# Performance work log

Measured on AMD Instinct MI355X. Metric: run time of the kernel, lower is better.

The kernel has to match this reference:

```python
import jax, jax.numpy as jnp
import numpy as np

LEAK = 0.2
TEMP = 0.1          # CausalMask temperature
SPARSITY_W = 0.1
MI_W = 0.01
DAG_W = 1.0

def _leaky(x):
    return jax.nn.leaky_relu(x, LEAK)

def setup_inputs() -> dict:
    key = jax.random.key(0)
    B, F, S, H = 4096, 512, 32, 512
    H2, CH = H // 2, 64
    P = S * (S - 1) // 2  # 496 MI estimators
    ks = jax.random.split(key, 32)
    def w(k, shape, fan_in):
        return jax.random.normal(k, shape, jnp.float32) / np.sqrt(fan_in)
    return {
        'features': jax.random.normal(ks[0], (B, F), jnp.float32),
        'eps':      jax.random.normal(ks[1], (B, S), jnp.float32),
        'enc_w1': w(ks[2], (F, H), F),   'enc_b1': w(ks[3], (H,), H),
        'enc_w2': w(ks[4], (H, 2 * S), H), 'enc_b2': w(ks[5], (2 * S,), H) * 0.1,
        'log_weight': jax.random.normal(ks[6], (S, S), jnp.float32) * 0.5,
        'mech_w1': w(ks[7], (S, S, H2), S), 'mech_b1': w(ks[8], (S, H2), H2),
        'mech_w2': w(ks[9], (S, H2), H2),   'mech_b2': w(ks[10], (S,), H2),
        'dec_w1': w(ks[11], (S, H), S),  'dec_b1': w(ks[12], (H,), H),
        'dec_w2': w(ks[13], (H, F), H),  'dec_b2': w(ks[14], (F,), H),
        'mi_w1': w(ks[15], (P, 2, CH), 2),  'mi_b1': w(ks[16], (P, CH), CH),
        'mi_w2': w(ks[17], (P, CH, CH), CH), 'mi_b2': w(ks[18], (P, CH), CH),
        'mi_w3': w(ks[19], (P, CH), CH),     'mi_b3': w(ks[20], (P,), CH),
    }

def _forward(features, eps, enc_w1, enc_b1, enc_w2, enc_b2, log_weight,
             mech_w1, mech_b1, mech_w2, mech_b2, dec_w1, dec_b1, dec_w2, dec_b2,
             mi_w1, mi_b1, mi_w2, mi_b2, mi_w3, mi_b3):
    S = log_weight.shape[0]
    # ---- encode ----
    h = _leaky(features @ enc_w1 + enc_b1)
    params = h @ enc_w2 + enc_b2
    mean, log_std = jnp.split(params, 2, axis=-1)
    std = jnp.exp(log_std)
    z = mean + std * eps                                   # [B,S]
    # ---- soft causal adjacency (training mode) ----
    eye = jnp.eye(S, dtype=features.dtype)
    upper = jnp.triu(jnp.ones((S, S), features.dtype), k=1)
    lw = log_weight * upper - 10.0 * eye
    A = jax.nn.sigmoid(lw / TEMP)                          # [S,S]
    # ---- apply_causal_structure: stoch_dim tiny MLPs, vectorized ----
    # z_parents[b,i,s] = z[b,s] * A[s,i]
    zp = z[:, None, :] * A.T[None, :, :]                   # [B,S,S]
    h1 = _leaky(jnp.einsum('bis,ish->bih', zp, mech_w1) + mech_b1)  # [B,S,H2]
    z_causal = jnp.einsum('bih,ih->bi', h1, mech_w2) + mech_b2      # [B,S]
    # ---- decode ----
    recon = _leaky(z_causal @ dec_w1 + dec_b1) @ dec_w2 + dec_b2    # [B,F]
    # ---- losses ----
    recon_loss = jnp.mean((recon - features) ** 2)
    kl_loss = 0.5 * jnp.sum(mean ** 2 + std ** 2 - 2.0 * log_std - 1.0, axis=-1).mean()
    Asig = jax.nn.sigmoid(log_weight)
    sparsity_loss = jnp.sum(jnp.abs(Asig))
    # MI: one tiny MLP per (i<j) pair, row-major order == torch loop order
    iu, ju = jnp.triu_indices(S, k=1)
    pair = jnp.stack([z[:, iu], z[:, ju]], axis=-1)        # [B,P,2]
    m1 = _leaky(jnp.einsum('bpi,pih->bph', pair, mi_w1) + mi_b1)
    m2 = _leaky(jnp.einsum('bph,phk->bpk', m1, mi_w2) + mi_b2)
    mi_est = (jnp.einsum('bph,ph->bp', m2, mi_w3) + mi_b3).mean(0)  # [P]
    mi_loss = jnp.sum(jax.nn.sigmoid(log_weight[iu, ju]) * mi_est)
    # DAG: truncated matrix-exponential trace penalty
    A2 = Asig * Asig
    expm = eye
    mp = eye
    fact = 1.0
    for i in range(1, 10):
        fact *= i
        mp = mp @ A2
        expm = expm + mp / fact
    dag_loss = (jnp.trace(expm) - S) ** 2
    total_loss = recon_loss + kl_loss + SPARSITY_W * sparsity_loss + MI_W * mi_loss + DAG_W * dag_loss
    return z_causal, mean, std, recon, total_loss, recon_loss, kl_loss, sparsity_loss, mi_loss, dag_loss

def reference(features, eps, enc_w1, enc_b1, enc_w2, enc_b2, log_weight,
              mech_w1, mech_b1, mech_w2, mech_b2, dec_w1, dec_b1, dec_w2, dec_b2,
              mi_w1, mi_b1, mi_w2, mi_b2, mi_w3, mi_b3):
    return _forward(features, eps, enc_w1, enc_b1, enc_w2, enc_b2, log_weight,
                    mech_w1, mech_b1, mech_w2, mech_b2, dec_w1, dec_b1, dec_w2, dec_b2,
                    mi_w1, mi_b1, mi_w2, mi_b2, mi_w3, mi_b3)
```

## Files before the change

kernel.cpp:

```cpp
#include <hip/hip_runtime.h>
#include <hip/hip_bf16.h>

typedef float f32x4 __attribute__((ext_vector_type(4)));
typedef short s16x8 __attribute__((ext_vector_type(8)));

__device__ __forceinline__ float leaky2(float x){ return fmaf(0.4f, fabsf(x), 0.6f * x); }

__device__ __forceinline__ short f2bf(float f){
    return __builtin_bit_cast(short, __float2bfloat16(f));
}

__global__ __launch_bounds__(256) void k_cvt(
    const float* __restrict__ feat, const float* __restrict__ ew1,
    const float* __restrict__ ew2, const float* __restrict__ dw2,
    const float* __restrict__ mw1, const float* __restrict__ mw2,
    short* __restrict__ featbf, short* __restrict__ w1p,
    short* __restrict__ ew2p, short* __restrict__ dw2p,
    short* __restrict__ mw1p, short* __restrict__ mw2p,
    const float* __restrict__ lw, float* __restrict__ A,
    float* __restrict__ acc)
{
    if (blockIdx.x >= 2048){
        __shared__ float A2s[1024], mp[1024], red[256];
        const int t = threadIdx.x;
        float part = 0.f;
        #pragma unroll
        for (int q = 0; q < 4; ++q){
            int e = t * 4 + q;
            int r = e >> 5, c = e & 31;
            float v = lw[e];
            float sig = 1.f / (1.f + expf(-v));
            float l2 = (r < c) ? v * 10.f : ((r == c) ? -100.f : 0.f);
            A[e] = 1.f / (1.f + expf(-l2));
            part += sig;
            float a2 = sig * sig;
            A2s[e] = a2; mp[e] = a2;
        }
        red[t] = part; __syncthreads();
        for (int s = 128; s > 0; s >>= 1){ if (t < s) red[t] += red[t + s]; __syncthreads(); }
        if (t == 0) acc[2] = red[0];

        const float invf[10] = {0.f, 1.f, 0.5f, 1.6666667e-1f, 4.1666667e-2f,
                                8.3333333e-3f, 1.3888889e-3f, 1.9841270e-4f,
                                2.4801587e-5f, 2.7557319e-6f};
        float tr = 0.f;
        const int r = t >> 3, c0 = (t & 7) * 4;
        for (int n = 1; n <= 9; ++n){
            __syncthreads();
            if (t == 0){
                float s = 0.f;
                for (int k2 = 0; k2 < 32; ++k2) s += mp[k2 * 33];
                tr += s * invf[n];
            }
            if (n == 9) break;
            float av[4] = {0.f, 0.f, 0.f, 0.f};
            for (int k2 = 0; k2 < 32; ++k2){
                float m = mp[r * 32 + k2];
                #pragma unroll
                for (int q = 0; q < 4; ++q) av[q] = fmaf(m, A2s[k2 * 32 + c0 + q], av[q]);
            }
            __syncthreads();
            #pragma unroll
            for (int q = 0; q < 4; ++q) mp[r * 32 + c0 + q] = av[q];
        }
        if (t == 0) acc[3] = tr * tr;
        return;
    }
    for (int idx = blockIdx.x * 256 + threadIdx.x; idx < 4947968; idx += 2048 * 256){
        if (idx < 2097152){ featbf[idx] = f2bf(feat[idx]); continue; }
        int s = idx - 2097152;
        if (s < 262144){
            int k = s >> 9, n = s & 511;
            int lane = (((k >> 3) & 3) << 4) | (n & 15);
            w1p[((n >> 4) * 16 + (k >> 5)) * 512 + lane * 8 + (k & 7)] = f2bf(ew1[s]);
            continue;
        }
        s -= 262144;
        if (s < 32768){
            int k = s >> 6, n = s & 63;
            int lane = (((k >> 3) & 3) << 4) | (n & 15);
            ew2p[((n >> 4) * 16 + (k >> 5)) * 512 + lane * 8 + (k & 7)] = f2bf(ew2[s]);
            continue;
        }
        s -= 32768;
        if (s < 262144){
            int k = s >> 9, n = s & 511;
            int lane = (((k >> 3) & 3) << 4) | (n & 15);
            dw2p[((n >> 4) * 16 + (k >> 5)) * 512 + lane * 8 + (k & 7)] = f2bf(dw2[s]);
            continue;
        }
        s -= 262144;
        if (s < 262144){
            int i = s >> 13, r2 = s & 8191;
            int k = r2 >> 8, n = r2 & 255;
            int lane = (((k >> 3) & 3) << 4) | (n & 15);
            mw1p[i * 8192 + (n >> 4) * 512 + lane * 8 + (k & 7)] = f2bf(mw1[s]);
            continue;
        }
        s -= 262144;
        int p = s >> 12, r2 = s & 4095;
        int k = r2 >> 6, n = r2 & 63;
        int lane = (((k >> 3) & 3) << 4) | (n & 15);
        mw2p[p * 4096 + ((n >> 4) * 2 + (k >> 5)) * 512 + lane * 8 + (k & 7)] = f2bf(mw2[s]);
    }
}

__global__ __launch_bounds__(256) void k_genc(const short* __restrict__ Abf,
                                              const short* __restrict__ Bp,
                                              const float* __restrict__ bias,
                                              short* __restrict__ Hbf)
{
    const int lane = threadIdx.x & 63, wv = threadIdx.x >> 6;
    const int ml = lane & 15, kg = lane >> 4;
    const int b0 = blockIdx.x * 32 + (wv >> 1) * 16;
    const int c0 = blockIdx.y * 128 + (wv & 1) * 64;
    const int nt0 = c0 >> 4;
    f32x4 acc[4] = {};
    for (int kt = 0; kt < 16; ++kt){
        s16x8 a = *(const s16x8*)&Abf[(size_t)(b0 + ml) * 512 + kt * 32 + kg * 8];
        #pragma unroll
        for (int ni = 0; ni < 4; ++ni){
            s16x8 b = *(const s16x8*)&Bp[((nt0 + ni) * 16 + kt) * 512 + lane * 8];
            acc[ni] = __builtin_amdgcn_mfma_f32_16x16x32_bf16(a, b, acc[ni], 0, 0, 0);
        }
    }
    #pragma unroll
    for (int ni = 0; ni < 4; ++ni){
        int col = c0 + ni * 16 + ml;
        float bv = bias[col];
        #pragma unroll
        for (int r = 0; r < 4; ++r){
            int row = b0 + kg * 4 + r;
            Hbf[(size_t)row * 512 + col] = f2bf(leaky2(acc[ni][r] + bv));
        }
    }
}

__global__ __launch_bounds__(256) void k_grec(const short* __restrict__ Abf,
                                              const short* __restrict__ Bp,
                                              const float* __restrict__ bias,
                                              const float* __restrict__ feat,
                                              float* __restrict__ recon,
                                              float* __restrict__ accg)
{
    __shared__ float red[256];
    const int t = threadIdx.x;
    const int lane = t & 63, wv = t >> 6;
    const int ml = lane & 15, kg = lane >> 4;
    const int b0 = blockIdx.x * 32 + (wv >> 1) * 16;
    const int c0 = blockIdx.y * 128 + (wv & 1) * 64;
    const int nt0 = c0 >> 4;
    f32x4 acc[4] = {};
    for (int kt = 0; kt < 16; ++kt){
        s16x8 a = *(const s16x8*)&Abf[(size_t)(b0 + ml) * 512 + kt * 32 + kg * 8];
        #pragma unroll
        for (int ni = 0; ni < 4; ++ni){
            s16x8 b = *(const s16x8*)&Bp[((nt0 + ni) * 16 + kt) * 512 + lane * 8];
            acc[ni] = __builtin_amdgcn_mfma_f32_16x16x32_bf16(a, b, acc[ni], 0, 0, 0);
        }
    }
    float lsum = 0.f;
    #pragma unroll
    for (int ni = 0; ni < 4; ++ni){
        int col = c0 + ni * 16 + ml;
        float bv = bias[col];
        #pragma unroll
        for (int r = 0; r < 4; ++r){
            int row = b0 + kg * 4 + r;
            float v = acc[ni][r] + bv;
            float d = v - feat[(size_t)row * 512 + col];
            lsum = fmaf(d, d, lsum);
            recon[(size_t)row * 512 + col] = v;
        }
    }
    red[t] = lsum; __syncthreads();
    for (int s = 128; s > 0; s >>= 1){ if (t < s) red[t] += red[t + s]; __syncthreads(); }
    if (t == 0) atomicAdd(accg + 1, red[0]);
}

__global__ __launch_bounds__(256) void k_pmfma(const short* __restrict__ Hbf,
                                               const short* __restrict__ Bp,
                                               const float* __restrict__ b2,
                                               const float* __restrict__ eps,
                                               float* __restrict__ omean,
                                               float* __restrict__ ostd,
                                               float* __restrict__ zt,
                                               float* __restrict__ accg)
{
    __shared__ float P[16][65];
    __shared__ float zs[16][33];
    __shared__ float red[256];
    const int t = threadIdx.x, lane = t & 63, wv = t >> 6;
    const int ml = lane & 15, kg = lane >> 4;
    const int b0 = blockIdx.x * 16;
    f32x4 acc = {};
    for (int kt = 0; kt < 16; ++kt){
        s16x8 b = *(const s16x8*)&Bp[(wv * 16 + kt) * 512 + lane * 8];
        s16x8 a = *(const s16x8*)&Hbf[(size_t)(b0 + ml) * 512 + kt * 32 + kg * 8];
        acc = __builtin_amdgcn_mfma_f32_16x16x32_bf16(a, b, acc, 0, 0, 0);
    }
    {
        int col = wv * 16 + ml;
        float bv = b2[col];
        #pragma unroll
        for (int r = 0; r < 4; ++r)
            P[kg * 4 + r][col] = acc[r] + bv;
    }
    __syncthreads();
    float klp = 0.f;
    #pragma unroll
    for (int q = 0; q < 2; ++q){
        int e = q * 256 + t;
        int row = e >> 5, n = e & 31;
        float mean = P[row][n], ls = P[row][n + 32];
        float sd = expf(ls);
        size_t o = (size_t)(b0 + row) * 32 + n;
        float z = fmaf(sd, eps[o], mean);
        omean[o] = mean; ostd[o] = sd;
        zs[row][n] = z;
        klp += mean * mean + sd * sd - 2.f * ls - 1.f;
    }
    __syncthreads();
    #pragma unroll
    for (int q = 0; q < 2; ++q){
        int e = q * 256 + t;
        int n = e >> 4, row = e & 15;
        zt[(size_t)n * 4096 + b0 + row] = zs[row][n];
    }
    red[t] = klp; __syncthreads();
    for (int s = 128; s > 0; s >>= 1){ if (t < s) red[t] += red[t + s]; __syncthreads(); }
    if (t == 0) atomicAdd(accg + 0, red[0]);
}

__global__ __launch_bounds__(256) void k_mi(
    const float* __restrict__ zt,
    const float* __restrict__ w1g, const float* __restrict__ b1g,
    const short* __restrict__ w2p, const float* __restrict__ b2g,
    const float* __restrict__ w3g, float* __restrict__ macc)
{
    const int lane = threadIdx.x & 63, wv = threadIdx.x >> 6;
    const int ml = lane & 15, kg = lane >> 4;
    const int p = blockIdx.x >> 2, bq = blockIdx.x & 3;
    int pi = 0, rem = p;
    while (rem >= 31 - pi){ rem -= 31 - pi; ++pi; }
    const int pj = pi + 1 + rem;

    const int zrow = wv * 16 + ml;
    const float* zi_b = zt + (size_t)pi * 4096 + bq * 1024 + zrow;
    const float* zj_b = zt + (size_t)pj * 4096 + bq * 1024 + zrow;

    float w10s[2][8], w11s[2][8], b1s[2][8];
    #pragma unroll
    for (int ks = 0; ks < 2; ++ks)
        #pragma unroll
        for (int i2 = 0; i2 < 8; ++i2){
            int h = ks * 32 + kg * 8 + i2;
            w10s[ks][i2] = 0.6f * w1g[p * 128 + h];
            w11s[ks][i2] = 0.6f * w1g[p * 128 + 64 + h];
            b1s[ks][i2]  = 0.6f * b1g[p * 64 + h];
        }
    s16x8 bfr[4][2];
    f32x4 b2c[4];
    #pragma unroll
    for (int nb = 0; nb < 4; ++nb){
        float bv = b2g[p * 64 + nb * 16 + ml];
        b2c[nb][0] = bv; b2c[nb][1] = bv; b2c[nb][2] = bv; b2c[nb][3] = bv;
        #pragma unroll
        for (int ks = 0; ks < 2; ++ks)
            bfr[nb][ks] = *(const s16x8*)&w2p[(size_t)p * 4096 + (nb * 2 + ks) * 512 + lane * 8];
    }
    float slin[4] = {0.f, 0.f, 0.f, 0.f}, sabs[4] = {0.f, 0.f, 0.f, 0.f};
    float zi_c = zi_b[0], zj_c = zj_b[0];
    #pragma unroll 1
    for (int tile = 0; tile < 16; ++tile){
        int nx = (tile < 15 ? tile + 1 : 15) * 64;
        float zi_n = zi_b[nx], zj_n = zj_b[nx];
        s16x8 af0, af1;
        #pragma unroll
        for (int i2 = 0; i2 < 8; ++i2){
            float m0 = fmaf(zi_c, w10s[0][i2], fmaf(zj_c, w11s[0][i2], b1s[0][i2]));
            m0 = fmaf(0.66666669f, fabsf(m0), m0);
            af0[i2] = f2bf(m0);
            float m1 = fmaf(zi_c, w10s[1][i2], fmaf(zj_c, w11s[1][i2], b1s[1][i2]));
            m1 = fmaf(0.66666669f, fabsf(m1), m1);
            af1[i2] = f2bf(m1);
        }
        #pragma unroll
        for (int nb = 0; nb < 4; ++nb){
            f32x4 d = __builtin_amdgcn_mfma_f32_16x16x32_bf16(af0, bfr[nb][0], b2c[nb], 0, 0, 0);
            d = __builtin_amdgcn_mfma_f32_16x16x32_bf16(af1, bfr[nb][1], d, 0, 0, 0);
            #pragma unroll
            for (int r2 = 0; r2 < 4; ++r2){
                slin[nb] += d[r2];
                sabs[nb] += fabsf(d[r2]);
            }
        }
        zi_c = zi_n; zj_c = zj_n;
    }
    float s = 0.f;
    #pragma unroll
    for (int nb = 0; nb < 4; ++nb){
        float w3 = w3g[p * 64 + nb * 16 + ml];
        s = fmaf(0.6f * w3, slin[nb], fmaf(0.4f * w3, sabs[nb], s));
    }
    #pragma unroll
    for (int off = 32; off; off >>= 1) s += __shfl_xor(s, off);
    if (lane == 0) atomicAdd(&macc[p], s);
}

__global__ __launch_bounds__(256) void k_mech(
    const float* __restrict__ zt, const float* __restrict__ A,
    const short* __restrict__ W1p, const float* __restrict__ mb1,
    const float* __restrict__ mw2, const float* __restrict__ mb2,
    float* __restrict__ out_zc)
{
    __shared__ float sA[32], sB1[256], sW2[256];
    const int t = threadIdx.x, lane = t & 63, wv = t >> 6;
    const int ml = lane & 15, kg = lane >> 4;
    const int i = blockIdx.y;
    const int b0 = blockIdx.x * 64 + wv * 16;
    if (t < 32) sA[t] = A[t * 32 + i];
    sB1[t] = mb1[i * 256 + t];
    sW2[t] = mw2[i * 256 + t];
    __syncthreads();
    float zv[8];
    #pragma unroll
    for (int q = 0; q < 8; ++q)
        zv[q] = zt[(size_t)(kg * 8 + q) * 4096 + b0 + ml];
    s16x8 af;
    #pragma unroll
    for (int q = 0; q < 8; ++q)
        af[q] = f2bf(zv[q] * sA[kg * 8 + q]);
    float s[4] = {0.f, 0.f, 0.f, 0.f};
    #pragma unroll
    for (int nt = 0; nt < 16; ++nt){
        s16x8 bf = *(const s16x8*)&W1p[i * 8192 + nt * 512 + lane * 8];
        int col = nt * 16 + ml;
        float b1v = sB1[col], w2v = sW2[col];
        f32x4 d;
        d[0] = b1v; d[1] = b1v; d[2] = b1v; d[3] = b1v;
        d = __builtin_amdgcn_mfma_f32_16x16x32_bf16(af, bf, d, 0, 0, 0);
        float w2a = 0.6f * w2v, w2b = 0.4f * w2v;
        #pragma unroll
        for (int r = 0; r < 4; ++r)
            s[r] = fmaf(w2a, d[r], fmaf(w2b, fabsf(d[r]), s[r]));
    }
    #pragma unroll
    for (int off = 1; off < 16; off <<= 1)
        #pragma unroll
        for (int r = 0; r < 4; ++r) s[r] += __shfl_xor(s[r], off);
    if (ml == 0){
        float bb = mb2[i];
        #pragma unroll
        for (int r = 0; r < 4; ++r){
            int b = b0 + kg * 4 + r;
            out_zc[(size_t)b * 32 + i] = s[r] + bb;
        }
    }
}

__global__ __launch_bounds__(256) void k_dec1(
    const float* __restrict__ zc, const float* __restrict__ w1,
    const float* __restrict__ b1, short* __restrict__ d1)
{
    int gid = blockIdx.x * 256 + threadIdx.x;
    int b = gid >> 9, hc = gid & 511;
    const f32x4* z4 = (const f32x4*)(zc + (size_t)b * 32);
    float a = b1[hc];
    #pragma unroll
    for (int q = 0; q < 8; ++q){
        f32x4 v = z4[q];
        a = fmaf(v[0], w1[(q * 4 + 0) * 512 + hc], a);
        a = fmaf(v[1], w1[(q * 4 + 1) * 512 + hc], a);
        a = fmaf(v[2], w1[(q * 4 + 2) * 512 + hc], a);
        a = fmaf(v[3], w1[(q * 4 + 3) * 512 + hc], a);
    }
    d1[(size_t)b * 512 + hc] = f2bf(leaky2(a));
}

__global__ void k_final(const float* __restrict__ acc, const float* __restrict__ lw,
                        const float* __restrict__ b3, float* __restrict__ outs)
{
    __shared__ float red[512];
    int t = threadIdx.x;
    float c = 0.f;
    if (t < 496){
        int pi = 0, rem = t;
        while (rem >= 31 - pi){ rem -= 31 - pi; ++pi; }
        int pj = pi + 1 + rem;
        float est = acc[4 + t] * (1.f / 4096.f) + b3[t];
        float w = 1.f / (1.f + expf(-lw[pi * 32 + pj]));
        c = w * est;
    }
    red[t] = c; __syncthreads();
    for (int s = 256; s > 0; s >>= 1){ if (t < s) red[t] += red[t + s]; __syncthreads(); }
    if (t == 0){
        float mi    = red[0];
        float recon = acc[1] * (1.f / (4096.f * 512.f));
        float kl    = 0.5f * acc[0] * (1.f / 4096.f);
        float sp    = acc[2], dag = acc[3];
        outs[0] = recon + kl + 0.1f * sp + 0.01f * mi + dag;
        outs[1] = recon; outs[2] = kl; outs[3] = sp; outs[4] = mi; outs[5] = dag;
    }
}

extern "C" void kernel_launch(void* const* d_in, const int* in_sizes, int n_in,
                              void* d_out, int out_size, void* d_ws, size_t ws_size,
                              hipStream_t stream)
{
    const float* features = (const float*)d_in[0];
    const float* eps      = (const float*)d_in[1];
    const float* enc_w1   = (const float*)d_in[2];
    const float* enc_b1   = (const float*)d_in[3];
    const float* enc_w2   = (const float*)d_in[4];
    const float* enc_b2   = (const float*)d_in[5];
    const float* log_w    = (const float*)d_in[6];
    const float* mech_w1  = (const float*)d_in[7];
    const float* mech_b1  = (const float*)d_in[8];
    const float* mech_w2  = (const float*)d_in[9];
    const float* mech_b2  = (const float*)d_in[10];
    const float* dec_w1   = (const float*)d_in[11];
    const float* dec_b1   = (const float*)d_in[12];
    const float* dec_w2   = (const float*)d_in[13];
    const float* dec_b2   = (const float*)d_in[14];
    const float* mi_w1    = (const float*)d_in[15];
    const float* mi_b1    = (const float*)d_in[16];
    const float* mi_w2    = (const float*)d_in[17];
    const float* mi_b2    = (const float*)d_in[18];
    const float* mi_w3    = (const float*)d_in[19];
    const float* mi_b3    = (const float*)d_in[20];

    float* W      = (float*)d_ws;
    float* zt     = W;
    float* Abuf   = W + 262144;
    float* accums = W + 263168;
    short* w1p    = (short*)(W + 263680);
    short* ew2p   = (short*)(W + 394752);
    short* dw2p   = (short*)(W + 411136);
    short* mw1p   = (short*)(W + 542208);
    short* d1bf   = (short*)(W + 673280);
    short* mw2p   = d1bf;
    float* out    = (float*)d_out;
    short* featbf = (short*)(out + 393216);
    short* hbf    = (short*)(out + 393216 + 1048576);

    hipMemsetAsync(accums, 0, 512 * sizeof(float), stream);
    k_cvt<<<2049, 256, 0, stream>>>(features, enc_w1, enc_w2, dec_w2, mech_w1, mi_w2,
                                    featbf, w1p, ew2p, dw2p, mw1p, mw2p,
                                    log_w, Abuf, accums);
    k_genc<<<dim3(128, 4), 256, 0, stream>>>(featbf, w1p, enc_b1, hbf);
    k_pmfma<<<256, 256, 0, stream>>>(hbf, ew2p, enc_b2, eps,
                                     out + 131072, out + 262144, zt, accums);
    k_mi<<<1984, 256, 0, stream>>>(zt, mi_w1, mi_b1, mw2p, mi_b2, mi_w3, accums + 4);
    k_mech<<<dim3(64, 32), 256, 0, stream>>>(zt, Abuf, mw1p, mech_b1, mech_w2, mech_b2, out);
    k_dec1<<<8192, 256, 0, stream>>>(out, dec_w1, dec_b1, d1bf);
    k_grec<<<dim3(128, 4), 256, 0, stream>>>(d1bf, dw2p, dec_b2, features,
                                             out + 393216, accums);
    k_final<<<1, 512, 0, stream>>>(accums, log_w, mi_b3, out + 2490368);
}
```

Before: 133.4 us.

## Fuse encoder GEMMs, merge MI and mechanism kernels, fuse decoder into MFMA kernel

Fuses the two encoder GEMMs into one kernel that keeps the hidden activations in swizzled LDS instead of round-tripping them through global memory. The MI estimator and causal-mechanism kernels are merged into one launch using block-index ranges. The decoder's scalar first layer is replaced by an MFMA layer over a prepacked bf16 dec_w1, fused with the second GEMM through LDS. The aim is fewer launches and less intermediate global traffic. In exchange, the fused encoder runs only 256 blocks with 8 accumulators per wave, which lowers parallelism, and the decoder recomputes the hidden layer once per column block (4x redundant).

```diff
diff --git a/kernel.cpp b/kernel.cpp
--- a/kernel.cpp
+++ b/kernel.cpp
@@ -2,6 +2,7 @@
 #include <hip/hip_bf16.h>
 
 typedef float f32x4 __attribute__((ext_vector_type(4)));
+typedef float f32x2 __attribute__((ext_vector_type(2)));
 typedef short s16x8 __attribute__((ext_vector_type(8)));
 
 __device__ __forceinline__ float leaky2(float x){ return fmaf(0.4f, fabsf(x), 0.6f * x); }
@@ -14,9 +15,11 @@
     const float* __restrict__ feat, const float* __restrict__ ew1,
     const float* __restrict__ ew2, const float* __restrict__ dw2,
     const float* __restrict__ mw1, const float* __restrict__ mw2,
+    const float* __restrict__ dw1,
     short* __restrict__ featbf, short* __restrict__ w1p,
     short* __restrict__ ew2p, short* __restrict__ dw2p,
     short* __restrict__ mw1p, short* __restrict__ mw2p,
+    short* __restrict__ dw1p,
     const float* __restrict__ lw, float* __restrict__ A,
     float* __restrict__ acc)
 {
@@ -66,7 +69,7 @@
         if (t == 0) acc[3] = tr * tr;
         return;
     }
-    for (int idx = blockIdx.x * 256 + threadIdx.x; idx < 4947968; idx += 2048 * 256){
+    for (int idx = blockIdx.x * 256 + threadIdx.x; idx < 4964352; idx += 2048 * 256){
         if (idx < 2097152){ featbf[idx] = f2bf(feat[idx]); continue; }
         int s = idx - 2097152;
         if (s < 262144){
@@ -98,113 +101,70 @@
             continue;
         }
         s -= 262144;
-        int p = s >> 12, r2 = s & 4095;
-        int k = r2 >> 6, n = r2 & 63;
+        if (s < 2031616){
+            int p = s >> 12, r2 = s & 4095;
+            int k = r2 >> 6, n = r2 & 63;
+            int lane = (((k >> 3) & 3) << 4) | (n & 15);
+            mw2p[p * 4096 + ((n >> 4) * 2 + (k >> 5)) * 512 + lane * 8 + (k & 7)] = f2bf(mw2[s]);
+            continue;
+        }
+        s -= 2031616;
+        int k = s >> 9, n = s & 511;
         int lane = (((k >> 3) & 3) << 4) | (n & 15);
-        mw2p[p * 4096 + ((n >> 4) * 2 + (k >> 5)) * 512 + lane * 8 + (k & 7)] = f2bf(mw2[s]);
-    }
-}
-
-__global__ __launch_bounds__(256) void k_genc(const short* __restrict__ Abf,
-                                              const short* __restrict__ Bp,
-                                              const float* __restrict__ bias,
-                                              short* __restrict__ Hbf)
-{
-    const int lane = threadIdx.x & 63, wv = threadIdx.x >> 6;
-    const int ml = lane & 15, kg = lane >> 4;
-    const int b0 = blockIdx.x * 32 + (wv >> 1) * 16;
-    const int c0 = blockIdx.y * 128 + (wv & 1) * 64;
-    const int nt0 = c0 >> 4;
-    f32x4 acc[4] = {};
-    for (int kt = 0; kt < 16; ++kt){
-        s16x8 a = *(const s16x8*)&Abf[(size_t)(b0 + ml) * 512 + kt * 32 + kg * 8];
-        #pragma unroll
-        for (int ni = 0; ni < 4; ++ni){
-            s16x8 b = *(const s16x8*)&Bp[((nt0 + ni) * 16 + kt) * 512 + lane * 8];
-            acc[ni] = __builtin_amdgcn_mfma_f32_16x16x32_bf16(a, b, acc[ni], 0, 0, 0);
-        }
-    }
-    #pragma unroll
-    for (int ni = 0; ni < 4; ++ni){
-        int col = c0 + ni * 16 + ml;
-        float bv = bias[col];
-        #pragma unroll
-        for (int r = 0; r < 4; ++r){
-            int row = b0 + kg * 4 + r;
-            Hbf[(size_t)row * 512 + col] = f2bf(leaky2(acc[ni][r] + bv));
-        }
-    }
-}
-
-__global__ __launch_bounds__(256) void k_grec(const short* __restrict__ Abf,
-                                              const short* __restrict__ Bp,
-                                              const float* __restrict__ bias,
-                                              const float* __restrict__ feat,
-                                              float* __restrict__ recon,
-                                              float* __restrict__ accg)
-{
-    __shared__ float red[256];
-    const int t = threadIdx.x;
-    const int lane = t & 63, wv = t >> 6;
-    const int ml = lane & 15, kg = lane >> 4;
-    const int b0 = blockIdx.x * 32 + (wv >> 1) * 16;
-    const int c0 = blockIdx.y * 128 + (wv & 1) * 64;
-    const int nt0 = c0 >> 4;
-    f32x4 acc[4] = {};
-    for (int kt = 0; kt < 16; ++kt){
-        s16x8 a = *(const s16x8*)&Abf[(size_t)(b0 + ml) * 512 + kt * 32 + kg * 8];
-        #pragma unroll
-        for (int ni = 0; ni < 4; ++ni){
-            s16x8 b = *(const s16x8*)&Bp[((nt0 + ni) * 16 + kt) * 512 + lane * 8];
-            acc[ni] = __builtin_amdgcn_mfma_f32_16x16x32_bf16(a, b, acc[ni], 0, 0, 0);
-        }
-    }
-    float lsum = 0.f;
-    #pragma unroll
-    for (int ni = 0; ni < 4; ++ni){
-        int col = c0 + ni * 16 + ml;
-        float bv = bias[col];
-        #pragma unroll
-        for (int r = 0; r < 4; ++r){
-            int row = b0 + kg * 4 + r;
-            float v = acc[ni][r] + bv;
-            float d = v - feat[(size_t)row * 512 + col];
-            lsum = fmaf(d, d, lsum);
-            recon[(size_t)row * 512 + col] = v;
-        }
-    }
-    red[t] = lsum; __syncthreads();
-    for (int s = 128; s > 0; s >>= 1){ if (t < s) red[t] += red[t + s]; __syncthreads(); }
-    if (t == 0) atomicAdd(accg + 1, red[0]);
-}
-
-__global__ __launch_bounds__(256) void k_pmfma(const short* __restrict__ Hbf,
-                                               const short* __restrict__ Bp,
-                                               const float* __restrict__ b2,
-                                               const float* __restrict__ eps,
-                                               float* __restrict__ omean,
-                                               float* __restrict__ ostd,
-                                               float* __restrict__ zt,
-                                               float* __restrict__ accg)
-{
+        dw1p[(n >> 4) * 512 + lane * 8 + (k & 7)] = f2bf(dw1[s]);
+    }
+}
+
+__global__ __launch_bounds__(256) void k_encf(
+    const short* __restrict__ featbf, const short* __restrict__ w1p,
+    const float* __restrict__ eb1, const short* __restrict__ ew2p,
+    const float* __restrict__ eb2, const float* __restrict__ eps,
+    float* __restrict__ omean, float* __restrict__ ostd,
+    float* __restrict__ zt, float* __restrict__ accg)
+{
+    __shared__ short hlds[8192];
     __shared__ float P[16][65];
     __shared__ float zs[16][33];
     __shared__ float red[256];
     const int t = threadIdx.x, lane = t & 63, wv = t >> 6;
     const int ml = lane & 15, kg = lane >> 4;
     const int b0 = blockIdx.x * 16;
-    f32x4 acc = {};
+
+    f32x4 acc1[8] = {};
     for (int kt = 0; kt < 16; ++kt){
-        s16x8 b = *(const s16x8*)&Bp[(wv * 16 + kt) * 512 + lane * 8];
-        s16x8 a = *(const s16x8*)&Hbf[(size_t)(b0 + ml) * 512 + kt * 32 + kg * 8];
-        acc = __builtin_amdgcn_mfma_f32_16x16x32_bf16(a, b, acc, 0, 0, 0);
+        s16x8 a = *(const s16x8*)&featbf[(size_t)(b0 + ml) * 512 + kt * 32 + kg * 8];
+        #pragma unroll
+        for (int nf = 0; nf < 8; ++nf){
+            s16x8 b = *(const s16x8*)&w1p[((wv * 8 + nf) * 16 + kt) * 512 + lane * 8];
+            acc1[nf] = __builtin_amdgcn_mfma_f32_16x16x32_bf16(a, b, acc1[nf], 0, 0, 0);
+        }
+    }
+    #pragma unroll
+    for (int nf = 0; nf < 8; ++nf){
+        int col = wv * 128 + nf * 16 + ml;
+        float bv = eb1[col];
+        #pragma unroll
+        for (int r = 0; r < 4; ++r){
+            int row = kg * 4 + r;
+            int byte = (row * 1024 + col * 2) ^ ((row & 7) << 4);
+            hlds[byte >> 1] = f2bf(leaky2(acc1[nf][r] + bv));
+        }
+    }
+    __syncthreads();
+
+    f32x4 acc2 = {};
+    for (int kt = 0; kt < 16; ++kt){
+        int byte = (ml * 1024 + kt * 64 + kg * 16) ^ ((ml & 7) << 4);
+        s16x8 a = *(const s16x8*)((const char*)hlds + byte);
+        s16x8 b = *(const s16x8*)&ew2p[(wv * 16 + kt) * 512 + lane * 8];
+        acc2 = __builtin_amdgcn_mfma_f32_16x16x32_bf16(a, b, acc2, 0, 0, 0);
     }
     {
         int col = wv * 16 + ml;
-        float bv = b2[col];
+        float bv = eb2[col];
         #pragma unroll
         for (int r = 0; r < 4; ++r)
-            P[kg * 4 + r][col] = acc[r] + bv;
+            P[kg * 4 + r][col] = acc2[r] + bv;
     }
     __syncthreads();
     float klp = 0.f;
@@ -232,150 +192,213 @@
     if (t == 0) atomicAdd(accg + 0, red[0]);
 }
 
-__global__ __launch_bounds__(256) void k_mi(
+__global__ __launch_bounds__(256) void k_mimech(
     const float* __restrict__ zt,
     const float* __restrict__ w1g, const float* __restrict__ b1g,
     const short* __restrict__ w2p, const float* __restrict__ b2g,
-    const float* __restrict__ w3g, float* __restrict__ macc)
-{
-    const int lane = threadIdx.x & 63, wv = threadIdx.x >> 6;
-    const int ml = lane & 15, kg = lane >> 4;
-    const int p = blockIdx.x >> 2, bq = blockIdx.x & 3;
-    int pi = 0, rem = p;
-    while (rem >= 31 - pi){ rem -= 31 - pi; ++pi; }
-    const int pj = pi + 1 + rem;
-
-    const int zrow = wv * 16 + ml;
-    const float* zi_b = zt + (size_t)pi * 4096 + bq * 1024 + zrow;
-    const float* zj_b = zt + (size_t)pj * 4096 + bq * 1024 + zrow;
-
-    float w10s[2][8], w11s[2][8], b1s[2][8];
-    #pragma unroll
-    for (int ks = 0; ks < 2; ++ks)
-        #pragma unroll
-        for (int i2 = 0; i2 < 8; ++i2){
-            int h = ks * 32 + kg * 8 + i2;
-            w10s[ks][i2] = 0.6f * w1g[p * 128 + h];
-            w11s[ks][i2] = 0.6f * w1g[p * 128 + 64 + h];
-            b1s[ks][i2]  = 0.6f * b1g[p * 64 + h];
-        }
-    s16x8 bfr[4][2];
-    f32x4 b2c[4];
-    #pragma unroll
-    for (int nb = 0; nb < 4; ++nb){
-        float bv = b2g[p * 64 + nb * 16 + ml];
-        b2c[nb][0] = bv; b2c[nb][1] = bv; b2c[nb][2] = bv; b2c[nb][3] = bv;
-        #pragma unroll
-        for (int ks = 0; ks < 2; ++ks)
-            bfr[nb][ks] = *(const s16x8*)&w2p[(size_t)p * 4096 + (nb * 2 + ks) * 512 + lane * 8];
-    }
-    float slin[4] = {0.f, 0.f, 0.f, 0.f}, sabs[4] = {0.f, 0.f, 0.f, 0.f};
-    float zi_c = zi_b[0], zj_c = zj_b[0];
-    #pragma unroll 1
-    for (int tile = 0; tile < 16; ++tile){
-        int nx = (tile < 15 ? tile + 1 : 15) * 64;
-        float zi_n = zi_b[nx], zj_n = zj_b[nx];
-        s16x8 af0, af1;
-        #pragma unroll
-        for (int i2 = 0; i2 < 8; ++i2){
-            float m0 = fmaf(zi_c, w10s[0][i2], fmaf(zj_c, w11s[0][i2], b1s[0][i2]));
-            m0 = fmaf(0.66666669f, fabsf(m0), m0);
-            af0[i2] = f2bf(m0);
-            float m1 = fmaf(zi_c, w10s[1][i2], fmaf(zj_c, w11s[1][i2], b1s[1][i2]));
-            m1 = fmaf(0.66666669f, fabsf(m1), m1);
-            af1[i2] = f2bf(m1);
-        }
-        #pragma unroll
-        for (int nb = 0; nb < 4; ++nb){
-            f32x4 d = __builtin_amdgcn_mfma_f32_16x16x32_bf16(af0, bfr[nb][0], b2c[nb], 0, 0, 0);
-            d = __builtin_amdgcn_mfma_f32_16x16x32_bf16(af1, bfr[nb][1], d, 0, 0, 0);
-            #pragma unroll
-            for (int r2 = 0; r2 < 4; ++r2){
-                slin[nb] += d[r2];
-                sabs[nb] += fabsf(d[r2]);
-            }
-        }
-        zi_c = zi_n; zj_c = zj_n;
-    }
-    float s = 0.f;
-    #pragma unroll
-    for (int nb = 0; nb < 4; ++nb){
-        float w3 = w3g[p * 64 + nb * 16 + ml];
-        s = fmaf(0.6f * w3, slin[nb], fmaf(0.4f * w3, sabs[nb], s));
-    }
-    #pragma unroll
-    for (int off = 32; off; off >>= 1) s += __shfl_xor(s, off);
-    if (lane == 0) atomicAdd(&macc[p], s);
-}
-
-__global__ __launch_bounds__(256) void k_mech(
-    const float* __restrict__ zt, const float* __restrict__ A,
-    const short* __restrict__ W1p, const float* __restrict__ mb1,
-    const float* __restrict__ mw2, const float* __restrict__ mb2,
-    float* __restrict__ out_zc)
+    const float* __restrict__ w3g, float* __restrict__ macc,
+    const float* __restrict__ A, const short* __restrict__ W1p,
+    const float* __restrict__ mb1, const float* __restrict__ mw2,
+    const float* __restrict__ mb2, float* __restrict__ out_zc)
 {
     __shared__ float sA[32], sB1[256], sW2[256];
     const int t = threadIdx.x, lane = t & 63, wv = t >> 6;
     const int ml = lane & 15, kg = lane >> 4;
-    const int i = blockIdx.y;
-    const int b0 = blockIdx.x * 64 + wv * 16;
-    if (t < 32) sA[t] = A[t * 32 + i];
-    sB1[t] = mb1[i * 256 + t];
-    sW2[t] = mw2[i * 256 + t];
+    if (blockIdx.x < 1984){
+        const int p = blockIdx.x >> 2, bq = blockIdx.x & 3;
+        int pi = 0, rem = p;
+        while (rem >= 31 - pi){ rem -= 31 - pi; ++pi; }
+        const int pj = pi + 1 + rem;
+
+        const int zrow = wv * 16 + ml;
+        const float* zi_b = zt + (size_t)pi * 4096 + bq * 1024 + zrow;
+        const float* zj_b = zt + (size_t)pj * 4096 + bq * 1024 + zrow;
+
+        f32x2 w10v[2][4], w11v[2][4], b1v[2][4];
+        #pragma unroll
+        for (int ks = 0; ks < 2; ++ks)
+            #pragma unroll
+            for (int q = 0; q < 4; ++q){
+                int h = ks * 32 + kg * 8 + q * 2;
+                w10v[ks][q] = *(const f32x2*)&w1g[p * 128 + h] * 0.6f;
+                w11v[ks][q] = *(const f32x2*)&w1g[p * 128 + 64 + h] * 0.6f;
+                b1v[ks][q]  = *(const f32x2*)&b1g[p * 64 + h] * 0.6f;
+            }
+        s16x8 bfr[4][2];
+        f32x4 b2c[4];
+        #pragma unroll
+        for (int nb = 0; nb < 4; ++nb){
+            float bv = b2g[p * 64 + nb * 16 + ml];
+            b2c[nb][0] = bv; b2c[nb][1] = bv; b2c[nb][2] = bv; b2c[nb][3] = bv;
+            #pragma unroll
+            for (int ks = 0; ks < 2; ++ks)
+                bfr[nb][ks] = *(const s16x8*)&w2p[(size_t)p * 4096 + (nb * 2 + ks) * 512 + lane * 8];
+        }
+        const f32x2 c23 = {0.66666669f, 0.66666669f};
+        float slin[4] = {0.f, 0.f, 0.f, 0.f}, sabs[4] = {0.f, 0.f, 0.f, 0.f};
+        #pragma unroll 1
+        for (int tile = 0; tile < 16; ++tile){
+            float zi_c = zi_b[tile * 64], zj_c = zj_b[tile * 64];
+            f32x2 zi2 = {zi_c, zi_c}, zj2 = {zj_c, zj_c};
+            s16x8 af0, af1;
+            #pragma unroll
+            for (int q = 0; q < 4; ++q){
+                f32x2 m0 = __builtin_elementwise_fma(zi2, w10v[0][q],
+                           __builtin_elementwise_fma(zj2, w11v[0][q], b1v[0][q]));
+                m0 = __builtin_elementwise_fma(c23, __builtin_elementwise_abs(m0), m0);
+                af0[q * 2] = f2bf(m0[0]); af0[q * 2 + 1] = f2bf(m0[1]);
+                f32x2 m1 = __builtin_elementwise_fma(zi2, w10v[1][q],
+                           __builtin_elementwise_fma(zj2, w11v[1][q], b1v[1][q]));
+                m1 = __builtin_elementwise_fma(c23, __builtin_elementwise_abs(m1), m1);
+                af1[q * 2] = f2bf(m1[0]); af1[q * 2 + 1] = f2bf(m1[1]);
+            }
+            #pragma unroll
+            for (int nb = 0; nb < 4; ++nb){
+                f32x4 d = __builtin_amdgcn_mfma_f32_16x16x32_bf16(af0, bfr[nb][0], b2c[nb], 0, 0, 0);
+                d = __builtin_amdgcn_mfma_f32_16x16x32_bf16(af1, bfr[nb][1], d, 0, 0, 0);
+                #pragma unroll
+                for (int r2 = 0; r2 < 4; ++r2){
+                    slin[nb] += d[r2];
+                    sabs[nb] += fabsf(d[r2]);
+                }
+            }
+        }
+        float s = 0.f;
+        #pragma unroll
+        for (int nb = 0; nb < 4; ++nb){
+            float w3 = w3g[p * 64 + nb * 16 + ml];
+            s = fmaf(0.6f * w3, slin[nb], fmaf(0.4f * w3, sabs[nb], s));
+        }
+        #pragma unroll
+        for (int off = 32; off; off >>= 1) s += __shfl_xor(s, off);
+        if (lane == 0) atomicAdd(&macc[p], s);
+    } else {
+        const int bx = blockIdx.x - 1984;
+        const int i = bx & 31;
+        const int b0 = (bx >> 5) * 64 + wv * 16;
+        if (t < 32) sA[t] = A[t * 32 + i];
+        sB1[t] = mb1[i * 256 + t];
+        sW2[t] = mw2[i * 256 + t];
+        __syncthreads();
+        float zv[8];
+        #pragma unroll
+        for (int q = 0; q < 8; ++q)
+            zv[q] = zt[(size_t)(kg * 8 + q) * 4096 + b0 + ml];
+        s16x8 af;
+        #pragma unroll
+        for (int q = 0; q < 8; ++q)
+            af[q] = f2bf(zv[q] * sA[kg * 8 + q]);
+        float s[4] = {0.f, 0.f, 0.f, 0.f};
+        #pragma unroll
+        for (int nt = 0; nt < 16; ++nt){
+            s16x8 bf = *(const s16x8*)&W1p[i * 8192 + nt * 512 + lane * 8];
+            int col = nt * 16 + ml;
+            float b1e = sB1[col], w2v = sW2[col];
+            f32x4 d;
+            d[0] = b1e; d[1] = b1e; d[2] = b1e; d[3] = b1e;
+            d = __builtin_amdgcn_mfma_f32_16x16x32_bf16(af, bf, d, 0, 0, 0);
+            float w2a = 0.6f * w2v, w2b = 0.4f * w2v;
+            #pragma unroll
+            for (int r = 0; r < 4; ++r)
+                s[r] = fmaf(w2a, d[r], fmaf(w2b, fabsf(d[r]), s[r]));
+        }
+        #pragma unroll
+        for (int off = 1; off < 16; off <<= 1)
+            #pragma unroll
+            for (int r = 0; r < 4; ++r) s[r] += __shfl_xor(s[r], off);
+        if (ml == 0){
+            float bb = mb2[i];
+            #pragma unroll
+            for (int r = 0; r < 4; ++r){
+                int b = b0 + kg * 4 + r;
+                out_zc[(size_t)b * 32 + i] = s[r] + bb;
+            }
+        }
+    }
+}
+
+__global__ __launch_bounds__(256) void k_decf(
+    const float* __restrict__ zc, const short* __restrict__ dw1p,
+    const float* __restrict__ db1, const short* __restrict__ dw2p,
+    const float* __restrict__ db2, const float* __restrict__ feat,
+    float* __restrict__ recon, float* __restrict__ accg)
+{
+    __shared__ short dlds[16384];
+    __shared__ float red[256];
+    const int t = threadIdx.x, lane = t & 63, wv = t >> 6;
+    const int ml = lane & 15, kg = lane >> 4;
+    const int b0 = blockIdx.x * 32;
+    const int c0 = blockIdx.y * 128;
+
+    s16x8 af[2];
+    #pragma unroll
+    for (int m = 0; m < 2; ++m){
+        int row = b0 + m * 16 + ml;
+        f32x4 z0 = *(const f32x4*)&zc[(size_t)row * 32 + kg * 8];
+        f32x4 z1 = *(const f32x4*)&zc[(size_t)row * 32 + kg * 8 + 4];
+        #pragma unroll
+        for (int e = 0; e < 4; ++e){
+            af[m][e] = f2bf(z0[e]);
+            af[m][e + 4] = f2bf(z1[e]);
+        }
+    }
+    #pragma unroll
+    for (int nf = 0; nf < 8; ++nf){
+        int nt = wv * 8 + nf;
+        s16x8 bf = *(const s16x8*)&dw1p[nt * 512 + lane * 8];
+        int col = nt * 16 + ml;
+        float b1e = db1[col];
+        f32x4 c; c[0] = b1e; c[1] = b1e; c[2] = b1e; c[3] = b1e;
+        #pragma unroll
+        for (int m = 0; m < 2; ++m){
+            f32x4 d = __builtin_amdgcn_mfma_f32_16x16x32_bf16(af[m], bf, c, 0, 0, 0);
+            #pragma unroll
+            for (int r = 0; r < 4; ++r){
+                int row = m * 16 + kg * 4 + r;
+                int byte = (row * 1024 + col * 2) ^ ((row & 7) << 4);
+                dlds[byte >> 1] = f2bf(leaky2(d[r]));
+            }
+        }
+    }
     __syncthreads();
-    float zv[8];
-    #pragma unroll
-    for (int q = 0; q < 8; ++q)
-        zv[q] = zt[(size_t)(kg * 8 + q) * 4096 + b0 + ml];
-    s16x8 af;
-    #pragma unroll
-    for (int q = 0; q < 8; ++q)
-        af[q] = f2bf(zv[q] * sA[kg * 8 + q]);
-    float s[4] = {0.f, 0.f, 0.f, 0.f};
-    #pragma unroll
-    for (int nt = 0; nt < 16; ++nt){
-        s16x8 bf = *(const s16x8*)&W1p[i * 8192 + nt * 512 + lane * 8];
-        int col = nt * 16 + ml;
-        float b1v = sB1[col], w2v = sW2[col];
-        f32x4 d;
-        d[0] = b1v; d[1] = b1v; d[2] = b1v; d[3] = b1v;
-        d = __builtin_amdgcn_mfma_f32_16x16x32_bf16(af, bf, d, 0, 0, 0);
-        float w2a = 0.6f * w2v, w2b = 0.4f * w2v;
-        #pragma unroll
-        for (int r = 0; r < 4; ++r)
-            s[r] = fmaf(w2a, d[r], fmaf(w2b, fabsf(d[r]), s[r]));
-    }
-    #pragma unroll
-    for (int off = 1; off < 16; off <<= 1)
-        #pragma unroll
-        for (int r = 0; r < 4; ++r) s[r] += __shfl_xor(s[r], off);
-    if (ml == 0){
-        float bb = mb2[i];
-        #pragma unroll
-        for (int r = 0; r < 4; ++r){
-            int b = b0 + kg * 4 + r;
-            out_zc[(size_t)b * 32 + i] = s[r] + bb;
-        }
-    }
-}
-
-__global__ __launch_bounds__(256) void k_dec1(
-    const float* __restrict__ zc, const float* __restrict__ w1,
-    const float* __restrict__ b1, short* __restrict__ d1)
-{
-    int gid = blockIdx.x * 256 + threadIdx.x;
-    int b = gid >> 9, hc = gid & 511;
-    const f32x4* z4 = (const f32x4*)(zc + (size_t)b * 32);
-    float a = b1[hc];
-    #pragma unroll
-    for (int q = 0; q < 8; ++q){
-        f32x4 v = z4[q];
-        a = fmaf(v[0], w1[(q * 4 + 0) * 512 + hc], a);
-        a = fmaf(v[1], w1[(q * 4 + 1) * 512 + hc], a);
-        a = fmaf(v[2], w1[(q * 4 + 2) * 512 + hc], a);
-        a = fmaf(v[3], w1[(q * 4 + 3) * 512 + hc], a);
-    }
-    d1[(size_t)b * 512 + hc] = f2bf(leaky2(a));
+
+    f32x4 acc[2][2] = {};
+    for (int kt = 0; kt < 16; ++kt){
+        s16x8 a[2];
+        #pragma unroll
+        for (int m = 0; m < 2; ++m){
+            int row = m * 16 + ml;
+            int byte = (row * 1024 + kt * 64 + kg * 16) ^ ((row & 7) << 4);
+            a[m] = *(const s16x8*)((const char*)dlds + byte);
+        }
+        #pragma unroll
+        for (int j = 0; j < 2; ++j){
+            int nt = (c0 >> 4) + wv * 2 + j;
+            s16x8 b = *(const s16x8*)&dw2p[(nt * 16 + kt) * 512 + lane * 8];
+            #pragma unroll
+            for (int m = 0; m < 2; ++m)
+                acc[m][j] = __builtin_amdgcn_mfma_f32_16x16x32_bf16(a[m], b, acc[m][j], 0, 0, 0);
+        }
+    }
+    float lsum = 0.f;
+    #pragma unroll
+    for (int j = 0; j < 2; ++j){
+        int col = c0 + (wv * 2 + j) * 16 + ml;
+        float bv = db2[col];
+        #pragma unroll
+        for (int m = 0; m < 2; ++m)
+            #pragma unroll
+            for (int r = 0; r < 4; ++r){
+                int row = b0 + m * 16 + kg * 4 + r;
+                float v = acc[m][j][r] + bv;
+                float d = v - feat[(size_t)row * 512 + col];
+                lsum = fmaf(d, d, lsum);
+                recon[(size_t)row * 512 + col] = v;
+            }
+    }
+    red[t] = lsum; __syncthreads();
+    for (int s = 128; s > 0; s >>= 1){ if (t < s) red[t] += red[t + s]; __syncthreads(); }
+    if (t == 0) atomicAdd(accg + 1, red[0]);
 }
 
 __global__ void k_final(const float* __restrict__ acc, const float* __restrict__ lw,
@@ -438,23 +461,20 @@
     short* ew2p   = (short*)(W + 394752);
     short* dw2p   = (short*)(W + 411136);
     short* mw1p   = (short*)(W + 542208);
-    short* d1bf   = (short*)(W + 673280);
-    short* mw2p   = d1bf;
+    short* mw2p   = (short*)(W + 673280);
+    short* dw1p   = (short*)(W + 1689088);
     float* out    = (float*)d_out;
     short* featbf = (short*)(out + 393216);
-    short* hbf    = (short*)(out + 393216 + 1048576);
 
     hipMemsetAsync(accums, 0, 512 * sizeof(float), stream);
     k_cvt<<<2049, 256, 0, stream>>>(features, enc_w1, enc_w2, dec_w2, mech_w1, mi_w2,
-                                    featbf, w1p, ew2p, dw2p, mw1p, mw2p,
+                                    dec_w1, featbf, w1p, ew2p, dw2p, mw1p, mw2p, dw1p,
                                     log_w, Abuf, accums);
-    k_genc<<<dim3(128, 4), 256, 0, stream>>>(featbf, w1p, enc_b1, hbf);
-    k_pmfma<<<256, 256, 0, stream>>>(hbf, ew2p, enc_b2, eps,
-                                     out + 131072, out + 262144, zt, accums);
-    k_mi<<<1984, 256, 0, stream>>>(zt, mi_w1, mi_b1, mw2p, mi_b2, mi_w3, accums + 4);
-    k_mech<<<dim3(64, 32), 256, 0, stream>>>(zt, Abuf, mw1p, mech_b1, mech_w2, mech_b2, out);
-    k_dec1<<<8192, 256, 0, stream>>>(out, dec_w1, dec_b1, d1bf);
-    k_grec<<<dim3(128, 4), 256, 0, stream>>>(d1bf, dw2p, dec_b2, features,
+    k_encf<<<256, 256, 0, stream>>>(featbf, w1p, enc_b1, ew2p, enc_b2, eps,
+                                    out + 131072, out + 262144, zt, accums);
+    k_mimech<<<4032, 256, 0, stream>>>(zt, mi_w1, mi_b1, mw2p, mi_b2, mi_w3, accums + 4,
+                                       Abuf, mw1p, mech_b1, mech_w2, mech_b2, out);
+    k_decf<<<dim3(128, 4), 256, 0, stream>>>(out, dw1p, dec_b1, dw2p, dec_b2, features,
                                              out + 393216, accums);
     k_final<<<1, 512, 0, stream>>>(accums, log_w, mi_b3, out + 2490368);
 }
```

Result: faster. 129.5 us (-3.0%).
